# Kernel optimization log

Hardware: AMD Instinct MI355X
Metric: run time of the kernel (lower is better)

Reference implementation:

```python
import jax, jax.numpy as jnp
import numpy as np

D_MODEL = 1024
N_DIM = 64      # per-head dim; scores scaled by 1/sqrt(n_dim)
N_HEADS = 16
SEQ = 4096
LN_EPS = 1e-5


def setup_inputs() -> dict:
    key = jax.random.key(0)
    ks = jax.random.split(key, 12)
    hd = N_HEADS * N_DIM  # == D_MODEL (required by residual add)
    s = 0.02
    return {
        "embed_word_vec": jax.random.normal(ks[0], (SEQ, D_MODEL), dtype=jnp.float32),
        "attn_mask": jax.random.uniform(ks[1], (SEQ, SEQ)) < 0.1,  # True = masked out
        "wq": jax.random.normal(ks[2], (D_MODEL, hd), dtype=jnp.float32) * s,
        "bq": jnp.zeros((hd,), dtype=jnp.float32),
        "wk": jax.random.normal(ks[3], (D_MODEL, hd), dtype=jnp.float32) * s,
        "bk": jnp.zeros((hd,), dtype=jnp.float32),
        "wv": jax.random.normal(ks[4], (D_MODEL, hd), dtype=jnp.float32) * s,
        "bv": jnp.zeros((hd,), dtype=jnp.float32),
        "wo": jax.random.normal(ks[5], (hd, D_MODEL), dtype=jnp.float32) * s,
        "bo": jnp.zeros((D_MODEL,), dtype=jnp.float32),
        "gamma": jnp.ones((D_MODEL,), dtype=jnp.float32),
        "beta": jnp.zeros((D_MODEL,), dtype=jnp.float32),
    }


def reference(embed_word_vec, attn_mask, wq, bq, wk, bk, wv, bv, wo, bo, gamma, beta):
    x = embed_word_vec                      # [S, d_model]
    q = x @ wq + bq                         # [S, H*D]
    k = x @ wk + bk
    v = x @ wv + bv
    scores = (q @ k.T) / jnp.sqrt(jnp.asarray(N_DIM, dtype=q.dtype))  # [S, S]
    scores = jnp.where(attn_mask, jnp.asarray(-jnp.inf, dtype=scores.dtype), scores)
    attention = jax.nn.softmax(scores, axis=-1)                       # [S, S]
    context = attention @ v + x             # AV + residual, [S, d_model]
    h = context @ wo + bo                   # out projection
    # LayerNorm over last dim
    mu = jnp.mean(h, axis=-1, keepdims=True)
    var = jnp.mean(jnp.square(h - mu), axis=-1, keepdims=True)
    output = (h - mu) * jax.lax.rsqrt(var + LN_EPS) * gamma + beta
    return (output, attention)
```

## Files before the change

kernel.cpp:

```cpp
#include <hip/hip_runtime.h>
#include <hip/hip_bf16.h>
#include <stdint.h>

#define SEQ 4096
#define DM  1024

typedef __attribute__((ext_vector_type(8))) short bf16x8;
typedef __attribute__((ext_vector_type(4))) float f32x4;

template <int V> struct Int { static constexpr int v = V; };

__device__ __forceinline__ short f2bf(float f) {
  union { float f; unsigned int i; } x; x.f = f;
  unsigned int r = x.i + 0x7FFFu + ((x.i >> 16) & 1u);
  return (short)(r >> 16);
}
__device__ __forceinline__ float bf2f(short s) {
  union { unsigned int i; float f; } u;
  u.i = ((unsigned int)(unsigned short)s) << 16;
  return u.f;
}

__device__ __forceinline__ void gload16(const short* g, short* l) {
  __builtin_amdgcn_global_load_lds(
      (const __attribute__((address_space(1))) unsigned int*)g,
      (__attribute__((address_space(3))) unsigned int*)l, 16, 0, 0);
}

__device__ __forceinline__ float wave_max(float v) {
#pragma unroll
  for (int o = 32; o; o >>= 1) v = fmaxf(v, __shfl_xor(v, o));
  return v;
}
__device__ __forceinline__ float wave_sum(float v) {
#pragma unroll
  for (int o = 32; o; o >>= 1) v += __shfl_xor(v, o);
  return v;
}

#define BARRIER() do { asm volatile("" ::: "memory"); \
  __builtin_amdgcn_s_barrier(); asm volatile("" ::: "memory"); } while (0)
#define MF(a, b, c) __builtin_amdgcn_mfma_f32_16x16x32_bf16(a, b, c, 0, 0, 0)

template <int EPI>
__global__ __launch_bounds__(512, 2) void gemm8(
    const short* __restrict__ A, const short* __restrict__ B,
    short* __restrict__ C, short* __restrict__ Cv,
    const float* __restrict__ bias, int Ksplit, int lda, int ldb, int ldc,
    int ldv, float scale, int ntm, int ntn, long csplit, int pc) {
  __shared__ short lds[2][4][8192];
  const int tid = threadIdx.x;
  const int lane = tid & 63;
  const int wid = tid >> 6;
  const int wr = wid >> 2;
  const int wc = wid & 3;
  const int bid = blockIdx.x, nwg = gridDim.x;
  const int chunk = nwg >> 3;
  const int wl = (bid & 7) * chunk + (bid >> 3);
  const int tpg = ntm * ntn;
  const int split = wl / tpg;
  const int r0 = wl - split * tpg;
  const int q = r0 / chunk, i0 = r0 % chunk;
  const int npatch = ntn / pc;
  const int m0 = ((q / npatch) * (chunk / pc) + i0 / pc) * 256;
  const int n0 = ((q % npatch) * pc + i0 % pc) * 256;
  const short* Ab = A + (long)split * Ksplit;
  const short* Bb = B + (long)split * Ksplit;
  short* Co = C + (long)split * csplit;

  const int o0 = tid * 16;
  const int oo = o0 ^ (((o0 >> 7) & 7) << 4);
  const int sr0 = oo >> 7;
  const int sc0 = (oo & 127) >> 1;

  auto stA = [&](int buf, int h, int kt) {
    const short* g = Ab + (long)(m0 + h * 128 + sr0) * lda + kt * 64 + sc0;
    short* l = &lds[buf][h][0] + wid * 512;
    gload16(g, l);
    gload16(g + (long)64 * lda, l + 4096);
  };
  auto stB = [&](int buf, int h, int kt) {
    const short* g = Bb + (long)(n0 + h * 128 + sr0) * ldb + kt * 64 + sc0;
    short* l = &lds[buf][2 + h][0] + wid * 512;
    gload16(g, l);
    gload16(g + (long)64 * ldb, l + 4096);
  };

  const int ll = lane & 15, lh = lane >> 4;
  auto ldaf = [&](int buf, int c, int mm, int kk) {
    const int r = c * 32 + mm * 16 + ll;
    const int off = (r * 64 + kk * 32 + lh * 8) ^ ((r & 7) << 3);
    return *(const bf16x8*)(&lds[buf][wr][0] + off);
  };
  auto ldbf = [&](int buf, int n, int kk) {
    const int r = (wc & 1) * 64 + n * 16 + ll;
    const int off = (r * 64 + kk * 32 + lh * 8) ^ ((r & 7) << 3);
    return *(const bf16x8*)(&lds[buf][2 + (wc >> 1)][0] + off);
  };

  f32x4 acc[8][4];
#pragma unroll
  for (int i = 0; i < 8; i++)
#pragma unroll
    for (int j = 0; j < 4; j++) acc[i][j] = (f32x4){0.f, 0.f, 0.f, 0.f};
  bf16x8 Bf[4][2];

  const int NT = Ksplit >> 6;
  stB(0, 0, 0); stB(0, 1, 0);
  stA(0, 0, 0); stA(0, 1, 0);
  stB(1, 0, 1); stB(1, 1, 1);
  asm volatile("s_waitcnt vmcnt(4)" ::: "memory");
  BARRIER();

  auto phase = [&](auto BUF, auto CC, auto LB, auto BARv, auto&& stg) {
    constexpr int buf = decltype(BUF)::v;
    constexpr int c = decltype(CC)::v;
    if constexpr (decltype(LB)::v != 0) {
#pragma unroll
      for (int n = 0; n < 4; n++) {
        Bf[n][0] = ldbf(buf, n, 0);
        Bf[n][1] = ldbf(buf, n, 1);
      }
    }
    bf16x8 a00 = ldaf(buf, c, 0, 0), a01 = ldaf(buf, c, 0, 1);
    bf16x8 a10 = ldaf(buf, c, 1, 0), a11 = ldaf(buf, c, 1, 1);
    stg();
    if constexpr (decltype(BARv)::v != 0) BARRIER();
    __builtin_amdgcn_s_setprio(1);
#pragma unroll
    for (int n = 0; n < 4; n++) {
      acc[2 * c][n] = MF(a00, Bf[n][0], acc[2 * c][n]);
      acc[2 * c][n] = MF(a01, Bf[n][1], acc[2 * c][n]);
      acc[2 * c + 1][n] = MF(a10, Bf[n][0], acc[2 * c + 1][n]);
      acc[2 * c + 1][n] = MF(a11, Bf[n][1], acc[2 * c + 1][n]);
    }
    __builtin_amdgcn_s_setprio(0);
  };

  for (int t = 0; t < NT; t += 2) {
    const bool nl = (t + 2 < NT);
    phase(Int<0>{}, Int<0>{}, Int<1>{}, Int<0>{},
          [&] { stA(1, 0, t + 1); stA(1, 1, t + 1); });
    phase(Int<0>{}, Int<1>{}, Int<0>{}, Int<1>{}, [] {});
    phase(Int<0>{}, Int<2>{}, Int<0>{}, Int<1>{},
          [&] { if (nl) { stB(0, 0, t + 2); stB(0, 1, t + 2); } });
    phase(Int<0>{}, Int<3>{}, Int<0>{}, Int<1>{}, [] {});
    if (nl) { asm volatile("s_waitcnt vmcnt(4)" ::: "memory"); }
    else    { asm volatile("s_waitcnt vmcnt(0)" ::: "memory"); }
    BARRIER();
    phase(Int<1>{}, Int<0>{}, Int<1>{}, Int<0>{},
          [&] { if (nl) { stA(0, 0, t + 2); stA(0, 1, t + 2); } });
    phase(Int<1>{}, Int<1>{}, Int<0>{}, Int<1>{}, [] {});
    phase(Int<1>{}, Int<2>{}, Int<0>{}, Int<1>{},
          [&] { if (nl) { stB(1, 0, t + 3); stB(1, 1, t + 3); } });
    phase(Int<1>{}, Int<3>{}, Int<0>{}, Int<1>{}, [] {});
    if (nl) {
      asm volatile("s_waitcnt vmcnt(4)" ::: "memory");
      BARRIER();
    }
  }

  const int rb = m0 + wr * 128 + lh * 4;
  const int cb0 = n0 + wc * 64 + ll;
  if (EPI == 3 && n0 >= 2048) {
#pragma unroll
    for (int mi = 0; mi < 8; mi++) {
#pragma unroll
      for (int n = 0; n < 4; n++) {
        const int col = cb0 + n * 16;
        const float bv = bias[col];
        short4 pk;
        pk.x = f2bf(acc[mi][n][0] + bv);
        pk.y = f2bf(acc[mi][n][1] + bv);
        pk.z = f2bf(acc[mi][n][2] + bv);
        pk.w = f2bf(acc[mi][n][3] + bv);
        *(short4*)(Cv + (long)(col - 2048) * ldv + rb + mi * 16) = pk;
      }
    }
    return;
  }
#pragma unroll
  for (int mi = 0; mi < 8; mi++) {
#pragma unroll
    for (int n = 0; n < 4; n++) {
      const int col = cb0 + n * 16;
      float bv = 0.f;
      if (EPI == 1 || EPI == 3) bv = bias[col];
#pragma unroll
      for (int r = 0; r < 4; r++) {
        const int row = rb + mi * 16 + r;
        const long off = (long)row * ldc + col;
        float v = acc[mi][n][r];
        if (EPI == 1 || EPI == 3) v += bv;
        if (EPI == 2) v *= scale;
        Co[off] = f2bf(v);
      }
    }
  }
}


__global__ __launch_bounds__(256) void cvt_f32_to_bf16(
    const float* __restrict__ in, short* __restrict__ out, int n4) {
  int i = blockIdx.x * 256 + threadIdx.x;
  if (i < n4) {
    float4 f = ((const float4*)in)[i];
    short4 o;
    o.x = f2bf(f.x); o.y = f2bf(f.y); o.z = f2bf(f.z); o.w = f2bf(f.w);
    ((short4*)out)[i] = o;
  }
}

__global__ void transpose_w4(const float* __restrict__ s0,
                             const float* __restrict__ s1,
                             const float* __restrict__ s2,
                             const float* __restrict__ s3,
                             short* __restrict__ d0, short* __restrict__ d1,
                             short* __restrict__ d2, short* __restrict__ d3) {
  const int z = blockIdx.z;
  const float* in = z == 0 ? s0 : z == 1 ? s1 : z == 2 ? s2 : s3;
  short* out = z == 0 ? d0 : z == 1 ? d1 : z == 2 ? d2 : d3;
  __shared__ float tile[32][33];
  const int bx = blockIdx.x * 32;
  const int by = blockIdx.y * 32;
  const int tx = threadIdx.x, ty = threadIdx.y;
#pragma unroll
  for (int i = 0; i < 32; i += 8)
    tile[ty + i][tx] = in[(long)(by + ty + i) * 1024 + bx + tx];
  __syncthreads();
#pragma unroll
  for (int i = 0; i < 32; i += 8)
    out[(long)(bx + ty + i) * 1024 + by + tx] = f2bf(tile[tx][ty + i]);
}

__global__ __launch_bounds__(256) void concat_bias(
    const float* __restrict__ bq, const float* __restrict__ bk,
    const float* __restrict__ bv, float* __restrict__ o) {
  int i = blockIdx.x * 256 + threadIdx.x;
  float v = (i < 1024) ? bq[i] : (i < 2048 ? bk[i - 1024] : bv[i - 2048]);
  o[i] = v;
}

__global__ __launch_bounds__(256) void softmax_rows(const short* __restrict__ Sb,
                                                    const int* __restrict__ mask,
                                                    short* __restrict__ Pb) {
  const long row = blockIdx.x;
  const bf16x8* src = (const bf16x8*)(Sb + row * SEQ);
  const int* mrow = mask + row * (long)SEQ;
  bf16x8* dst = (bf16x8*)(Pb + row * SEQ);
  const int tid = threadIdx.x;
  const int wid = tid >> 6, lane = tid & 63;
  bf16x8 a = src[tid], b = src[tid + 256];
  int4 ma0 = *(const int4*)(mrow + tid * 8);
  int4 ma1 = *(const int4*)(mrow + tid * 8 + 4);
  int4 mb0 = *(const int4*)(mrow + 2048 + tid * 8);
  int4 mb1 = *(const int4*)(mrow + 2048 + tid * 8 + 4);
  float v[16];
#pragma unroll
  for (int j = 0; j < 8; j++) { v[j] = bf2f(a[j]); v[8 + j] = bf2f(b[j]); }
  const int* mm0 = (const int*)&ma0;
  const int* mm1 = (const int*)&ma1;
  const int* mm2 = (const int*)&mb0;
  const int* mm3 = (const int*)&mb1;
#pragma unroll
  for (int j = 0; j < 4; j++) {
    if (mm0[j]) v[j] = -INFINITY;
    if (mm1[j]) v[4 + j] = -INFINITY;
    if (mm2[j]) v[8 + j] = -INFINITY;
    if (mm3[j]) v[12 + j] = -INFINITY;
  }
  float mx = -INFINITY;
#pragma unroll
  for (int j = 0; j < 16; j++) mx = fmaxf(mx, v[j]);
  mx = wave_max(mx);
  __shared__ float red[4];
  if (lane == 0) red[wid] = mx;
  __syncthreads();
  mx = fmaxf(fmaxf(red[0], red[1]), fmaxf(red[2], red[3]));
  float sum = 0.f;
#pragma unroll
  for (int j = 0; j < 16; j++) {
    v[j] = __expf(v[j] - mx);
    sum += v[j];
  }
  sum = wave_sum(sum);
  __shared__ float red2[4];
  if (lane == 0) red2[wid] = sum;
  __syncthreads();
  sum = red2[0] + red2[1] + red2[2] + red2[3];
  const float inv = 1.0f / sum;
  bf16x8 o0, o1;
#pragma unroll
  for (int j = 0; j < 8; j++) {
    o0[j] = f2bf(v[j] * inv);
    o1[j] = f2bf(v[8 + j] * inv);
  }
  dst[tid] = o0;
  dst[tid + 256] = o1;
}

__global__ __launch_bounds__(256) void expand_bf16_f32(
    const short* __restrict__ in, float* __restrict__ out) {
  long i = (long)blockIdx.x * 256 + threadIdx.x;
  bf16x8 a = ((const bf16x8*)in)[i];
  float4 lo, hi;
  lo.x = bf2f(a[0]); lo.y = bf2f(a[1]); lo.z = bf2f(a[2]); lo.w = bf2f(a[3]);
  hi.x = bf2f(a[4]); hi.y = bf2f(a[5]); hi.z = bf2f(a[6]); hi.w = bf2f(a[7]);
  ((float4*)out)[2 * i] = lo;
  ((float4*)out)[2 * i + 1] = hi;
}

__global__ __launch_bounds__(256) void reduce_ctx4(
    const short* __restrict__ p, const float* __restrict__ x,
    short* __restrict__ cb) {
  const long i = (long)blockIdx.x * 256 + threadIdx.x;
  bf16x8 a = ((const bf16x8*)p)[i];
  bf16x8 b = ((const bf16x8*)(p + 4194304))[i];
  bf16x8 c = ((const bf16x8*)(p + 8388608))[i];
  bf16x8 d = ((const bf16x8*)(p + 12582912))[i];
  float4 x0 = ((const float4*)x)[2 * i];
  float4 x1 = ((const float4*)x)[2 * i + 1];
  float xs[8] = {x0.x, x0.y, x0.z, x0.w, x1.x, x1.y, x1.z, x1.w};
  bf16x8 o;
#pragma unroll
  for (int j = 0; j < 8; j++)
    o[j] = f2bf(bf2f(a[j]) + bf2f(b[j]) + bf2f(c[j]) + bf2f(d[j]) + xs[j]);
  ((bf16x8*)cb)[i] = o;
}

__global__ __launch_bounds__(256) void ln4(
    const short* __restrict__ ph, const float* __restrict__ bo,
    const float* __restrict__ gamma, const float* __restrict__ beta,
    float* __restrict__ out) {
  const long row = blockIdx.x;
  const int tid = threadIdx.x;
  const int wid = tid >> 6, lane = tid & 63;
  const long base = row * DM + tid * 4;
  short4 p0 = *(const short4*)(ph + base);
  short4 p1 = *(const short4*)(ph + 4194304 + base);
  short4 p2 = *(const short4*)(ph + 8388608 + base);
  short4 p3 = *(const short4*)(ph + 12582912 + base);
  float4 bb = *(const float4*)(bo + tid * 4);
  float v[4];
  v[0] = bf2f(p0.x) + bf2f(p1.x) + bf2f(p2.x) + bf2f(p3.x) + bb.x;
  v[1] = bf2f(p0.y) + bf2f(p1.y) + bf2f(p2.y) + bf2f(p3.y) + bb.y;
  v[2] = bf2f(p0.z) + bf2f(p1.z) + bf2f(p2.z) + bf2f(p3.z) + bb.z;
  v[3] = bf2f(p0.w) + bf2f(p1.w) + bf2f(p2.w) + bf2f(p3.w) + bb.w;
  float s = v[0] + v[1] + v[2] + v[3];
  s = wave_sum(s);
  __shared__ float red[4];
  if (lane == 0) red[wid] = s;
  __syncthreads();
  const float mu = (red[0] + red[1] + red[2] + red[3]) * (1.f / DM);
  float var = 0.f;
#pragma unroll
  for (int j = 0; j < 4; j++) {
    float d = v[j] - mu;
    var += d * d;
  }
  var = wave_sum(var);
  __shared__ float red2[4];
  if (lane == 0) red2[wid] = var;
  __syncthreads();
  var = (red2[0] + red2[1] + red2[2] + red2[3]) * (1.f / DM);
  const float inv = rsqrtf(var + 1e-5f);
  float4 g = *(const float4*)(gamma + tid * 4);
  float4 be = *(const float4*)(beta + tid * 4);
  float4 o;
  o.x = (v[0] - mu) * inv * g.x + be.x;
  o.y = (v[1] - mu) * inv * g.y + be.y;
  o.z = (v[2] - mu) * inv * g.z + be.z;
  o.w = (v[3] - mu) * inv * g.w + be.w;
  *(float4*)(out + base) = o;
}

extern "C" void kernel_launch(void* const* d_in, const int* in_sizes, int n_in,
                              void* d_out, int out_size, void* d_ws,
                              size_t ws_size, hipStream_t stream) {
  const float* x    = (const float*)d_in[0];
  const int* mask   = (const int*)d_in[1];
  const float* wq   = (const float*)d_in[2];
  const float* bq   = (const float*)d_in[3];
  const float* wk   = (const float*)d_in[4];
  const float* bk   = (const float*)d_in[5];
  const float* wv   = (const float*)d_in[6];
  const float* bv   = (const float*)d_in[7];
  const float* wo   = (const float*)d_in[8];
  const float* bo   = (const float*)d_in[9];
  const float* gamma = (const float*)d_in[10];
  const float* beta  = (const float*)d_in[11];

  float* out  = (float*)d_out;
  float* attn = out + 4194304;
  short* Sb   = (short*)attn;
  short* pav  = (short*)attn;
  short* ph   = (short*)(attn + 8388608);
  short* cbuf = (short*)out;

  char* w = (char*)d_ws;
  short* wqkvT = (short*)(w + 0);
  short* woT   = (short*)(w + 6291456);
  short* xb    = (short*)(w + 8388608);
  short* qkv   = (short*)(w + 16777216);
  short* attnb = (short*)(w + 8388608);
  short* vT    = (short*)(w + 41943040);
  float* bqkv  = (float*)(w + 50331648);

  cvt_f32_to_bf16<<<4096, 256, 0, stream>>>(x, xb, 1048576);
  transpose_w4<<<dim3(32, 32, 4), dim3(32, 8), 0, stream>>>(
      wq, wk, wv, wo, wqkvT, wqkvT + 1048576, wqkvT + 2097152, woT);
  concat_bias<<<12, 256, 0, stream>>>(bq, bk, bv, bqkv);

  gemm8<3><<<192, 512, 0, stream>>>(xb, wqkvT, qkv, vT, bqkv,
                                    1024, 1024, 1024, 3072, 4096, 1.f,
                                    16, 12, 0, 6);

  gemm8<2><<<256, 512, 0, stream>>>(qkv, qkv + 1024, Sb, nullptr, nullptr,
                                    1024, 3072, 3072, 4096, 0, 0.125f,
                                    16, 16, 0, 8);

  softmax_rows<<<SEQ, 256, 0, stream>>>(Sb, mask, attnb);

  gemm8<0><<<256, 512, 0, stream>>>(attnb, vT, pav, nullptr, nullptr,
                                    1024, 4096, 4096, 1024, 0, 1.f,
                                    16, 4, 4194304L, 4);

  reduce_ctx4<<<2048, 256, 0, stream>>>(pav, x, cbuf);

  gemm8<0><<<256, 512, 0, stream>>>(cbuf, woT, ph, nullptr, nullptr,
                                    256, 1024, 1024, 1024, 0, 1.f,
                                    16, 4, 4194304L, 4);

  ln4<<<SEQ, 256, 0, stream>>>(ph, bo, gamma, beta, out);

  expand_bf16_f32<<<8192, 256, 0, stream>>>(attnb, attn);
}
```

Before: 196.8 us.

## Fuse fp32 attention output write into softmax, dropping separate expand pass

The softmax kernel now writes the fp32 attention matrix directly, alongside the bf16 copy used by the AV GEMM. This removes the final expand_bf16_f32 pass, which re-read the bf16 probabilities and wrote 64MB of fp32. To make it safe, the score buffer is moved into the upper half of each attention row (row stride 8192 shorts), and partial-AV and out-projection buffers are relocated to workspace. The fused path is only taken when the workspace is large enough, otherwise the old path runs.

Result: no change. 195.8 us (-0.5%).

```diff
diff --git a/kernel.cpp b/kernel.cpp
--- a/kernel.cpp
+++ b/kernel.cpp
@@ -241,11 +241,14 @@
   o[i] = v;
 }
 
+template <int FUSED>
 __global__ __launch_bounds__(256) void softmax_rows(const short* __restrict__ Sb,
                                                     const int* __restrict__ mask,
-                                                    short* __restrict__ Pb) {
+                                                    short* __restrict__ Pb,
+                                                    float* __restrict__ Af,
+                                                    int ld) {
   const long row = blockIdx.x;
-  const bf16x8* src = (const bf16x8*)(Sb + row * SEQ);
+  const bf16x8* src = (const bf16x8*)(Sb + row * ld);
   const int* mrow = mask + row * (long)SEQ;
   bf16x8* dst = (bf16x8*)(Pb + row * SEQ);
   const int tid = threadIdx.x;
@@ -292,11 +295,20 @@
   bf16x8 o0, o1;
 #pragma unroll
   for (int j = 0; j < 8; j++) {
-    o0[j] = f2bf(v[j] * inv);
-    o1[j] = f2bf(v[8 + j] * inv);
+    v[j] *= inv;
+    v[8 + j] *= inv;
+    o0[j] = f2bf(v[j]);
+    o1[j] = f2bf(v[8 + j]);
   }
   dst[tid] = o0;
   dst[tid + 256] = o1;
+  if (FUSED) {
+    float* orow = Af + row * (long)SEQ;
+    *(float4*)(orow + tid * 8) = (float4){v[0], v[1], v[2], v[3]};
+    *(float4*)(orow + tid * 8 + 4) = (float4){v[4], v[5], v[6], v[7]};
+    *(float4*)(orow + 2048 + tid * 8) = (float4){v[8], v[9], v[10], v[11]};
+    *(float4*)(orow + 2048 + tid * 8 + 4) = (float4){v[12], v[13], v[14], v[15]};
+  }
 }
 
 __global__ __launch_bounds__(256) void expand_bf16_f32(
@@ -392,19 +404,22 @@
 
   float* out  = (float*)d_out;
   float* attn = out + 4194304;
-  short* Sb   = (short*)attn;
-  short* pav  = (short*)attn;
-  short* ph   = (short*)(attn + 8388608);
   short* cbuf = (short*)out;
 
   char* w = (char*)d_ws;
+  const bool fused = ws_size >= (size_t)83886080 + 16384;
+  short* Sb   = fused ? (short*)attn + 4096 : (short*)attn;
+  const int ldS = fused ? 8192 : 4096;
+  short* pav  = fused ? (short*)(w + 50331648) : (short*)attn;
+  short* phh  = fused ? pav : (short*)(attn + 8388608);
+  float* bqkv = fused ? (float*)(w + 83886080) : (float*)(w + 50331648);
+
   short* wqkvT = (short*)(w + 0);
   short* woT   = (short*)(w + 6291456);
   short* xb    = (short*)(w + 8388608);
   short* qkv   = (short*)(w + 16777216);
   short* attnb = (short*)(w + 8388608);
   short* vT    = (short*)(w + 41943040);
-  float* bqkv  = (float*)(w + 50331648);
 
   cvt_f32_to_bf16<<<4096, 256, 0, stream>>>(x, xb, 1048576);
   transpose_w4<<<dim3(32, 32, 4), dim3(32, 8), 0, stream>>>(
@@ -416,10 +431,13 @@
                                     16, 12, 0, 6);
 
   gemm8<2><<<256, 512, 0, stream>>>(qkv, qkv + 1024, Sb, nullptr, nullptr,
-                                    1024, 3072, 3072, 4096, 0, 0.125f,
+                                    1024, 3072, 3072, ldS, 0, 0.125f,
                                     16, 16, 0, 8);
 
-  softmax_rows<<<SEQ, 256, 0, stream>>>(Sb, mask, attnb);
+  if (fused)
+    softmax_rows<1><<<SEQ, 256, 0, stream>>>(Sb, mask, attnb, attn, ldS);
+  else
+    softmax_rows<0><<<SEQ, 256, 0, stream>>>(Sb, mask, attnb, attn, ldS);
 
   gemm8<0><<<256, 512, 0, stream>>>(attnb, vT, pav, nullptr, nullptr,
                                     1024, 4096, 4096, 1024, 0, 1.f,
@@ -427,11 +445,11 @@
 
   reduce_ctx4<<<2048, 256, 0, stream>>>(pav, x, cbuf);
 
-  gemm8<0><<<256, 512, 0, stream>>>(cbuf, woT, ph, nullptr, nullptr,
+  gemm8<0><<<256, 512, 0, stream>>>(cbuf, woT, phh, nullptr, nullptr,
                                     256, 1024, 1024, 1024, 0, 1.f,
                                     16, 4, 4194304L, 4);
 
-  ln4<<<SEQ, 256, 0, stream>>>(ph, bo, gamma, beta, out);
-
-  expand_bf16_f32<<<8192, 256, 0, stream>>>(attnb, attn);
-}
+  ln4<<<SEQ, 256, 0, stream>>>(phh, bo, gamma, beta, out);
+
+  if (!fused) expand_bf16_f32<<<8192, 256, 0, stream>>>(attnb, attn);
+}
```
